# Optimization experiments

Measured on AMD Instinct MI355X. Metric: run time of the kernel, lower is better.

Reference implementation:

```python
import jax, jax.numpy as jnp
import numpy as np

B, L, D, H = 8, 1024, 512, 8
EPS = 1e-5

def setup_inputs() -> dict:
    key = jax.random.key(0)
    ks = jax.random.split(key, 12)
    s = lambda fan_in: 1.0 / np.sqrt(fan_in)
    u = lambda k, shape, sc: jax.random.uniform(k, shape, jnp.float32, -sc, sc)
    return {
        "input": jax.random.normal(ks[0], (B, L, D), jnp.float32),
        "wq": u(ks[1], (D, H * D), s(D)), "bq": u(ks[2], (H * D,), s(D)),
        "wk": u(ks[3], (D, H * D), s(D)), "bk": u(ks[4], (H * D,), s(D)),
        "wv": u(ks[5], (D, H * D), s(D)), "bv": u(ks[6], (H * D,), s(D)),
        "score_w": u(ks[7], (2 * D, 1), s(2 * D)), "score_b": u(ks[8], (1,), s(2 * D)),
        "fc_w": u(ks[9], (H * D, D), s(H * D)), "fc_b": u(ks[10], (D,), s(H * D)),
        "ln_g": jnp.ones((D,), jnp.float32), "ln_b": jnp.zeros((D,), jnp.float32),
    }

def reference(input, wq, bq, wk, bk, wv, bv, score_w, score_b, fc_w, fc_b, ln_g, ln_b):
    x = input
    b, l, d = x.shape
    h = wq.shape[1] // d
    # project and fold heads into leading batch dim: (h*b, l, d)
    def proj(w, bias):
        y = (x @ w + bias).reshape(b, l, h, d)
        return y.transpose(2, 0, 1, 3).reshape(h * b, l, d)
    q = proj(wq, bq)
    k = proj(wk, bk)
    v = proj(wv, bv)
    # _score(cat(k_i, q_j)) decomposed: k part uses score_w[:d], q part score_w[d:]
    sk = (k @ score_w[:d])[:, :, 0]   # (h*b, l) -> row index i
    sq = (q @ score_w[d:])[:, :, 0]   # (h*b, l) -> col index j
    kq = jnp.tanh(sk[:, :, None] + sq[:, None, :] + score_b[0])  # (h*b, l, l)
    # faithful to original bug: softmax over trailing size-1 dim -> all ones
    score = jax.nn.softmax(kq[..., None], axis=-1)[..., 0]       # (h*b, l, l)
    out = jnp.einsum('nij,njd->nid', score, v)                   # (h*b, l, d)
    out = out.reshape(h, b, l, d).transpose(1, 2, 0, 3).reshape(b, l, h * d)
    out = out @ fc_w + fc_b
    y = out + x
    mu = jnp.mean(y, axis=-1, keepdims=True)
    var = jnp.var(y, axis=-1, keepdims=True)
    return (y - mu) / jnp.sqrt(var + EPS) * ln_g + ln_b
```

## Files before the change

### kernel.cpp

```cpp
#include <hip/hip_runtime.h>

#define BB 8
#define LL 1024
#define DD 512
#define HDIM 4096
#define EPS_LN 1e-5f
#define NB 256
#define NT 1024
#define POISON_I ((int)0xAAAAAAAAu)


__device__ __forceinline__ void batch_bar(int* cnt) {
    asm volatile("s_waitcnt vmcnt(0)" ::: "memory");
    __syncthreads();
    if (threadIdx.x == 0) {
        __hip_atomic_fetch_add(cnt, 1, __ATOMIC_RELAXED,
                               __HIP_MEMORY_SCOPE_AGENT);
        while (__hip_atomic_load(cnt, __ATOMIC_RELAXED,
                                 __HIP_MEMORY_SCOPE_AGENT) !=
               POISON_I + 32)
            __builtin_amdgcn_s_sleep(1);
        asm volatile("" ::: "memory");
    }
    __syncthreads();
}

__global__ __launch_bounds__(NT) void mha_fused(
    const float* __restrict__ x,
    const float* __restrict__ wv,
    const float* __restrict__ bv,
    const float* __restrict__ fcw,
    const float* __restrict__ fcb,
    const float* __restrict__ g,
    const float* __restrict__ beta,
    float* __restrict__ out,
    float* __restrict__ xs,
    float* __restrict__ u,
    int* __restrict__ bar)
{
    __shared__ float redA[16][DD];
    __shared__ float xs_b[DD];
    __shared__ float Tpart[8][128];
    __shared__ float T_l[128];
    __shared__ float uf[DD];

    const int tid = threadIdx.x;
    const int bi  = blockIdx.x;
    const int b   = bi >> 5;
    const int j   = bi & 31;

    const int dv   = tid & 63;
    const int rowg = tid >> 6;
    float4 xa0, xa1, xb0, xb1;

    {
        const float* basep = x + ((size_t)(bi * 32 + rowg * 2)) * DD + dv * 8;
        xa0 = *(const float4*)(basep);
        xa1 = *(const float4*)(basep + 4);
        xb0 = *(const float4*)(basep + DD);
        xb1 = *(const float4*)(basep + DD + 4);

        float4* dst = (float4*)&redA[rowg][dv * 8];
        dst[0] = make_float4(xa0.x + xb0.x, xa0.y + xb0.y,
                             xa0.z + xb0.z, xa0.w + xb0.w);
        dst[1] = make_float4(xa1.x + xb1.x, xa1.y + xb1.y,
                             xa1.z + xb1.z, xa1.w + xb1.w);
        __syncthreads();

        if (tid < DD) {
            float s = 0.f;
#pragma unroll
            for (int gg = 0; gg < 16; ++gg) s += redA[gg][tid];
            atomicAdd(&xs[b * DD + tid], s);
        }
    }

    batch_bar(bar + b * 32);

    {
        const int c0 = j * 128;
        if (tid < DD) xs_b[tid] = xs[b * DD + tid];
        __syncthreads();

        const int cI = tid & 127;
        const int kg = tid >> 7;
        float t = 0.f;
        const float* wcol = wv + c0 + cI;
#pragma unroll 8
        for (int i = 0; i < 64; ++i) {
            const int k = kg * 64 + i;
            t += xs_b[k] * wcol[(size_t)k * HDIM];
        }
        Tpart[kg][cI] = t;
        __syncthreads();

        if (tid < 128) {
            float s = 0.f;
#pragma unroll
            for (int q = 0; q < 8; ++q) s += Tpart[q][tid];
            T_l[tid] = s + 1024.f * bv[c0 + tid];
        }
        __syncthreads();

        const int dd = tid & 511;
        const int ch = tid >> 9;
        float a = 0.f;
#pragma unroll 8
        for (int i = 0; i < 64; ++i) {
            const int c = ch * 64 + i;
            a += T_l[c] * fcw[(size_t)(c0 + c) * DD + dd];
        }
        atomicAdd(&u[b * DD + dd], a);
    }

    batch_bar(bar + (8 + b) * 32);

    {
        if (tid < DD) uf[tid] = u[b * DD + tid] + fcb[tid];
        __syncthreads();

        const int lane = dv;
        float4 uq0 = *(const float4*)(uf + lane * 8);
        float4 uq1 = *(const float4*)(uf + lane * 8 + 4);
        float4 g0 = *(const float4*)(g + lane * 8);
        float4 g1 = *(const float4*)(g + lane * 8 + 4);
        float4 b0 = *(const float4*)(beta + lane * 8);
        float4 b1 = *(const float4*)(beta + lane * 8 + 4);

#pragma unroll
        for (int it = 0; it < 2; ++it) {
            const int row = bi * 32 + rowg * 2 + it;
            const size_t off = (size_t)row * DD + lane * 8;
            float4 x0 = (it == 0) ? xa0 : xb0;
            float4 x1 = (it == 0) ? xa1 : xb1;

            float y[8];
            y[0] = x0.x + uq0.x;  y[1] = x0.y + uq0.y;
            y[2] = x0.z + uq0.z;  y[3] = x0.w + uq0.w;
            y[4] = x1.x + uq1.x;  y[5] = x1.y + uq1.y;
            y[6] = x1.z + uq1.z;  y[7] = x1.w + uq1.w;

            float s1 = 0.f, ss = 0.f;
#pragma unroll
            for (int i = 0; i < 8; ++i) { s1 += y[i]; ss += y[i] * y[i]; }
#pragma unroll
            for (int m = 1; m < 64; m <<= 1) {
                s1 += __shfl_xor(s1, m, 64);
                ss += __shfl_xor(ss, m, 64);
            }
            const float mean = s1 * (1.f / 512.f);
            const float var  = ss * (1.f / 512.f) - mean * mean;
            const float rstd = rsqrtf(var + EPS_LN);

            float4 o0, o1;
            o0.x = (y[0] - mean) * rstd * g0.x + b0.x;
            o0.y = (y[1] - mean) * rstd * g0.y + b0.y;
            o0.z = (y[2] - mean) * rstd * g0.z + b0.z;
            o0.w = (y[3] - mean) * rstd * g0.w + b0.w;
            o1.x = (y[4] - mean) * rstd * g1.x + b1.x;
            o1.y = (y[5] - mean) * rstd * g1.y + b1.y;
            o1.z = (y[6] - mean) * rstd * g1.z + b1.z;
            o1.w = (y[7] - mean) * rstd * g1.w + b1.w;
            *(float4*)(out + off)     = o0;
            *(float4*)(out + off + 4) = o1;
        }
    }
}

extern "C" void kernel_launch(void* const* d_in, const int* in_sizes, int n_in,
                              void* d_out, int out_size, void* d_ws, size_t ws_size,
                              hipStream_t stream) {
    const float* x   = (const float*)d_in[0];
    const float* wv  = (const float*)d_in[5];
    const float* bv  = (const float*)d_in[6];
    const float* fcw = (const float*)d_in[9];
    const float* fcb = (const float*)d_in[10];
    const float* lng = (const float*)d_in[11];
    const float* lnb = (const float*)d_in[12];

    float* xs  = (float*)d_ws;
    int*   bar = (int*)((char*)d_ws + 16 * 1024);
    float* u   = (float*)((char*)d_ws + 32 * 1024);
    float* out = (float*)d_out;

    mha_fused<<<NB, NT, 0, stream>>>(x, wv, bv, fcw, fcb, lng, lnb,
                                     out, xs, u, bar);
}
```

Measured before the change: 118.3 us.

## Double grid to 512 blocks of 512 threads and prefetch weights before barrier

Splits work across 512 blocks of 512 threads (64 per batch), each block handling 16 rows and 64 value-projection columns. Most of the wv column slice (48 of 64 per thread) is loaded into registers before the first grid barrier, and LayerNorm params and fc bias are loaded before the second, so global load latency overlaps barrier waiting. The barrier arrival count doubles to 64, and the large register array raises register pressure under the 4-blocks launch bound.

```diff
diff --git a/kernel.cpp b/kernel.cpp
--- a/kernel.cpp
+++ b/kernel.cpp
@@ -5,9 +5,10 @@
 #define DD 512
 #define HDIM 4096
 #define EPS_LN 1e-5f
-#define NB 256
-#define NT 1024
+#define NB 512
+#define NT 512
 #define POISON_I ((int)0xAAAAAAAAu)
+#define ARRIVALS 64
 
 
 __device__ __forceinline__ void batch_bar(int* cnt) {
@@ -18,14 +19,14 @@
                                __HIP_MEMORY_SCOPE_AGENT);
         while (__hip_atomic_load(cnt, __ATOMIC_RELAXED,
                                  __HIP_MEMORY_SCOPE_AGENT) !=
-               POISON_I + 32)
+               POISON_I + ARRIVALS)
             __builtin_amdgcn_s_sleep(1);
         asm volatile("" ::: "memory");
     }
     __syncthreads();
 }
 
-__global__ __launch_bounds__(NT) void mha_fused(
+__global__ __launch_bounds__(NT, 4) void mha_fused(
     const float* __restrict__ x,
     const float* __restrict__ wv,
     const float* __restrict__ bv,
@@ -38,27 +39,36 @@
     float* __restrict__ u,
     int* __restrict__ bar)
 {
-    __shared__ float redA[16][DD];
+    __shared__ float redA[8][DD];
     __shared__ float xs_b[DD];
-    __shared__ float Tpart[8][128];
-    __shared__ float T_l[128];
+    __shared__ float Tpart[8][64];
+    __shared__ float T_l[64];
     __shared__ float uf[DD];
 
     const int tid = threadIdx.x;
     const int bi  = blockIdx.x;
-    const int b   = bi >> 5;
-    const int j   = bi & 31;
+    const int b   = bi >> 6;
+    const int j   = bi & 63;
 
     const int dv   = tid & 63;
     const int rowg = tid >> 6;
+    const int cI = dv;
+    const int kg = rowg;
+
     float4 xa0, xa1, xb0, xb1;
+    float  wpre[48];
 
+    const float* wcol = wv + (size_t)(j * 64) + cI;
     {
-        const float* basep = x + ((size_t)(bi * 32 + rowg * 2)) * DD + dv * 8;
+        const float* basep = x + ((size_t)(bi * 16 + rowg * 2)) * DD + dv * 8;
         xa0 = *(const float4*)(basep);
         xa1 = *(const float4*)(basep + 4);
         xb0 = *(const float4*)(basep + DD);
         xb1 = *(const float4*)(basep + DD + 4);
+
+#pragma unroll
+        for (int i = 0; i < 48; ++i)
+            wpre[i] = wcol[(size_t)(kg * 64 + i) * HDIM];
 
         float4* dst = (float4*)&redA[rowg][dv * 8];
         dst[0] = make_float4(xa0.x + xb0.x, xa0.y + xb0.y,
@@ -67,70 +77,63 @@
                              xa1.z + xb1.z, xa1.w + xb1.w);
         __syncthreads();
 
-        if (tid < DD) {
-            float s = 0.f;
+        float s = 0.f;
 #pragma unroll
-            for (int gg = 0; gg < 16; ++gg) s += redA[gg][tid];
-            atomicAdd(&xs[b * DD + tid], s);
-        }
+        for (int gg = 0; gg < 8; ++gg) s += redA[gg][tid];
+        atomicAdd(&xs[b * DD + tid], s);
     }
 
     batch_bar(bar + b * 32);
 
     {
-        const int c0 = j * 128;
-        if (tid < DD) xs_b[tid] = xs[b * DD + tid];
+        xs_b[tid] = xs[b * DD + tid];
         __syncthreads();
 
-        const int cI = tid & 127;
-        const int kg = tid >> 7;
         float t = 0.f;
-        const float* wcol = wv + c0 + cI;
-#pragma unroll 8
-        for (int i = 0; i < 64; ++i) {
-            const int k = kg * 64 + i;
-            t += xs_b[k] * wcol[(size_t)k * HDIM];
-        }
+#pragma unroll
+        for (int i = 0; i < 48; ++i)
+            t += xs_b[kg * 64 + i] * wpre[i];
+#pragma unroll
+        for (int i = 48; i < 64; ++i)
+            t += xs_b[kg * 64 + i] * wcol[(size_t)(kg * 64 + i) * HDIM];
         Tpart[kg][cI] = t;
         __syncthreads();
 
-        if (tid < 128) {
+        if (tid < 64) {
             float s = 0.f;
 #pragma unroll
             for (int q = 0; q < 8; ++q) s += Tpart[q][tid];
-            T_l[tid] = s + 1024.f * bv[c0 + tid];
+            T_l[tid] = s + 1024.f * bv[j * 64 + tid];
         }
         __syncthreads();
 
-        const int dd = tid & 511;
-        const int ch = tid >> 9;
         float a = 0.f;
+        const float* frow = fcw + (size_t)(j * 64) * DD + tid;
 #pragma unroll 8
-        for (int i = 0; i < 64; ++i) {
-            const int c = ch * 64 + i;
-            a += T_l[c] * fcw[(size_t)(c0 + c) * DD + dd];
-        }
-        atomicAdd(&u[b * DD + dd], a);
+        for (int c = 0; c < 64; ++c)
+            a += T_l[c] * frow[(size_t)c * DD];
+        atomicAdd(&u[b * DD + tid], a);
     }
+
+    float4 g0  = *(const float4*)(g + dv * 8);
+    float4 g1  = *(const float4*)(g + dv * 8 + 4);
+    float4 bt0 = *(const float4*)(beta + dv * 8);
+    float4 bt1 = *(const float4*)(beta + dv * 8 + 4);
+    float  fpre = fcb[tid];
 
     batch_bar(bar + (8 + b) * 32);
 
     {
-        if (tid < DD) uf[tid] = u[b * DD + tid] + fcb[tid];
+        uf[tid] = u[b * DD + tid] + fpre;
         __syncthreads();
 
-        const int lane = dv;
-        float4 uq0 = *(const float4*)(uf + lane * 8);
-        float4 uq1 = *(const float4*)(uf + lane * 8 + 4);
-        float4 g0 = *(const float4*)(g + lane * 8);
-        float4 g1 = *(const float4*)(g + lane * 8 + 4);
-        float4 b0 = *(const float4*)(beta + lane * 8);
-        float4 b1 = *(const float4*)(beta + lane * 8 + 4);
+        float4 uq0 = *(const float4*)(uf + dv * 8);
+        float4 uq1 = *(const float4*)(uf + dv * 8 + 4);
 
 #pragma unroll
         for (int it = 0; it < 2; ++it) {
-            const int row = bi * 32 + rowg * 2 + it;
-            const size_t off = (size_t)row * DD + lane * 8;
+            const int row = bi * 16 + rowg * 2 + it;
+            const size_t off = (size_t)row * DD + dv * 8;
             float4 x0 = (it == 0) ? xa0 : xb0;
             float4 x1 = (it == 0) ? xa1 : xb1;
 
@@ -153,14 +156,14 @@
             const float rstd = rsqrtf(var + EPS_LN);
 
             float4 o0, o1;
-            o0.x = (y[0] - mean) * rstd * g0.x + b0.x;
-            o0.y = (y[1] - mean) * rstd * g0.y + b0.y;
-            o0.z = (y[2] - mean) * rstd * g0.z + b0.z;
-            o0.w = (y[3] - mean) * rstd * g0.w + b0.w;
-            o1.x = (y[4] - mean) * rstd * g1.x + b1.x;
-            o1.y = (y[5] - mean) * rstd * g1.y + b1.y;
-            o1.z = (y[6] - mean) * rstd * g1.z + b1.z;
-            o1.w = (y[7] - mean) * rstd * g1.w + b1.w;
+            o0.x = (y[0] - mean) * rstd * g0.x + bt0.x;
+            o0.y = (y[1] - mean) * rstd * g0.y + bt0.y;
+            o0.z = (y[2] - mean) * rstd * g0.z + bt0.z;
+            o0.w = (y[3] - mean) * rstd * g0.w + bt0.w;
+            o1.x = (y[4] - mean) * rstd * g1.x + bt1.x;
+            o1.y = (y[5] - mean) * rstd * g1.y + bt1.y;
+            o1.z = (y[6] - mean) * rstd * g1.z + bt1.z;
+            o1.w = (y[7] - mean) * rstd * g1.w + bt1.w;
             *(float4*)(out + off)     = o0;
             *(float4*)(out + off + 4) = o1;
         }
```

Measured after the change: 140.2 us. 1.19x slower.
